# Kernel tuning notes

Hardware: AMD Instinct MI355X
Metric: run time of the kernel (lower is better)

## Reference

```python
import jax, jax.numpy as jnp
import numpy as np

N_STATE = 4      # d_state from CrossMambaFusionBlock(d_state=4)
DT_RANK = 48     # ceil(768/16), standard Mamba dt_rank='auto'
D_CONV = 4       # depthwise causal conv kernel size


def _ln(x, g, b):
    m = jnp.mean(x, axis=-1, keepdims=True)
    v = jnp.mean((x - m) ** 2, axis=-1, keepdims=True)
    return (x - m) * jax.lax.rsqrt(v + 1e-5) * g + b


def _dwconv1d(u, w, b):
    # u: (B,L,D); w: (D,1,K) depthwise causal conv along token dim L
    K = w.shape[-1]
    up = jnp.pad(jnp.transpose(u, (0, 2, 1)), ((0, 0), (0, 0), (K - 1, 0)))
    out = jax.lax.conv_general_dilated(up, w, (1,), 'VALID',
                                       feature_group_count=w.shape[0],
                                       dimension_numbers=('NCH', 'OIH', 'NCH'))
    return jnp.transpose(out, (0, 2, 1)) + b


def _pre(x, g, b, Win, Wconv, bconv, Wxp, Wdt, bdt):
    # LayerNorm -> in_proj -> depthwise conv + SiLU -> dt/B/C projections
    B_, H, W, C = x.shape
    xn = _ln(x, g, b).reshape(B_, H * W, C)
    u, z = jnp.split(xn @ Win, 2, axis=-1)              # (B,L,D) each
    u = jax.nn.silu(_dwconv1d(u, Wconv, bconv))
    dbl = u @ Wxp                                        # (B,L,R+2N)
    dtr, Bm, Cm = jnp.split(dbl, [DT_RANK, DT_RANK + N_STATE], axis=-1)
    dt = jax.nn.softplus(dtr @ Wdt + bdt)                # (B,L,D)
    return u, z, dt, Bm, Cm


def _selective_scan(u, dt, Alog, Bm, Cm, Dskip):
    # u, dt: (B,L,D); Alog: (D,N); Bm, Cm: (B,L,N)
    A = -jnp.exp(Alog)
    dA = jnp.exp(dt[..., None] * A)                      # (B,L,D,N) decay
    dBu = (dt * u)[..., None] * Bm[:, :, None, :]        # (B,L,D,N) input

    def comb(c1, c2):
        a1, h1 = c1
        a2, h2 = c2
        return a1 * a2, a2 * h1 + h2

    _, h = jax.lax.associative_scan(comb, (dA, dBu), axis=1)
    return jnp.einsum('bldn,bln->bld', h, Cm) + u * Dskip


def _forward(x1, x2,
             ln_g1, ln_b1, Win1, Wconv1, bconv1, Wxp1, Wdt1, bdt1, Alog1, Dskip1, Wout1,
             ln_g2, ln_b2, Win2, Wconv2, bconv2, Wxp2, Wdt2, bdt2, Alog2, Dskip2, Wout2):
    x1 = jnp.transpose(x1, (0, 2, 3, 1))  # BCHW -> BHWC (as in forward_features)
    x2 = jnp.transpose(x2, (0, 2, 3, 1))
    B_, H, W, C = x1.shape
    u1, z1, dt1, B1, C1 = _pre(x1, ln_g1, ln_b1, Win1, Wconv1, bconv1, Wxp1, Wdt1, bdt1)
    u2, z2, dt2, B2, C2 = _pre(x2, ln_g2, ln_b2, Win2, Wconv2, bconv2, Wxp2, Wdt2, bdt2)
    # Cross-modal fusion: each stream's SSM state is read out with the OTHER
    # stream's C projection (cross selective scan).
    y1 = _selective_scan(u1, dt1, Alog1, B1, C2, Dskip1)
    y2 = _selective_scan(u2, dt2, Alog2, B2, C1, Dskip2)
    o1 = ((y1 * jax.nn.silu(z1)) @ Wout1).reshape(B_, H, W, C)
    o2 = ((y2 * jax.nn.silu(z2)) @ Wout2).reshape(B_, H, W, C)
    return x1 + o1, x2 + o2


def setup_inputs():
    key = jax.random.key(0)
    ks = jax.random.split(key, 16)
    B_, C, H, W = 2, 768, 64, 64
    D = C  # d_inner (ssm_ratio = 1)

    def nrm(k, shape, s=0.02):
        return jax.random.normal(k, shape, jnp.float32) * s

    inp = {
        'x1': jax.random.normal(ks[0], (B_, C, H, W), jnp.float32),
        'x2': jax.random.normal(ks[1], (B_, C, H, W), jnp.float32),
    }
    for i, o in ((1, 2), (2, 8)):
        inp[f'ln_g{i}'] = jnp.ones((C,), jnp.float32)
        inp[f'ln_b{i}'] = jnp.zeros((C,), jnp.float32)
        inp[f'Win{i}'] = nrm(ks[o], (C, 2 * D))
        inp[f'Wconv{i}'] = nrm(ks[o + 1], (D, 1, D_CONV), 0.1)
        inp[f'bconv{i}'] = jnp.zeros((D,), jnp.float32)
        inp[f'Wxp{i}'] = nrm(ks[o + 2], (D, DT_RANK + 2 * N_STATE))
        inp[f'Wdt{i}'] = nrm(ks[o + 3], (DT_RANK, D), 0.05)
        inp[f'bdt{i}'] = jnp.full((D,), -4.6, jnp.float32)  # softplus -> dt ~ 0.01
        inp[f'Alog{i}'] = jnp.log(jnp.broadcast_to(
            jnp.arange(1, N_STATE + 1, dtype=jnp.float32), (D, N_STATE)))
        inp[f'Dskip{i}'] = jnp.ones((D,), jnp.float32)
        inp[f'Wout{i}'] = nrm(ks[o + 4], (D, C))
    return inp


def reference(x1, x2,
              ln_g1, ln_b1, Win1, Wconv1, bconv1, Wxp1, Wdt1, bdt1, Alog1, Dskip1, Wout1,
              ln_g2, ln_b2, Win2, Wconv2, bconv2, Wxp2, Wdt2, bdt2, Alog2, Dskip2, Wout2):
    return _forward(x1, x2,
                    ln_g1, ln_b1, Win1, Wconv1, bconv1, Wxp1, Wdt1, bdt1, Alog1, Dskip1, Wout1,
                    ln_g2, ln_b2, Win2, Wconv2, bconv2, Wxp2, Wdt2, bdt2, Alog2, Dskip2, Wout2)
```

## Files before the change

kernel.cpp:

```cpp
#include <hip/hip_runtime.h>
#include <cmath>

#define LDIM 4096
#define CDIM 768
#define BDIM 2
#define NST 4
#define RNK 48
#define CH 64
#define LC 64
#define NDT 896

typedef short bf16x8 __attribute__((ext_vector_type(8)));
typedef float f32x4 __attribute__((ext_vector_type(4)));

__device__ __forceinline__ float sigmoidf_(float x) { return 1.f / (1.f + __expf(-x)); }

__device__ __forceinline__ unsigned short f2bf(float f) {
    unsigned int u = __float_as_uint(f);
    u += 0x7fffu + ((u >> 16) & 1u);
    return (unsigned short)(u >> 16);
}
__device__ __forceinline__ float bf2f(unsigned short us) {
    unsigned int u = ((unsigned int)us) << 16;
    return __uint_as_float(u);
}

__device__ __forceinline__ void llds16(const unsigned short* g, unsigned short* l) {
    __builtin_amdgcn_global_load_lds(
        (const __attribute__((address_space(1))) unsigned int*)g,
        (__attribute__((address_space(3))) unsigned int*)l, 16, 0, 0);
}

__global__ __launch_bounds__(256) void prep_kernel(
    const float* __restrict__ x0, const float* __restrict__ x1, float* __restrict__ stats,
    const float* __restrict__ Win0, const float* __restrict__ Win1,
    const float* __restrict__ Wout0, const float* __restrict__ Wout1,
    unsigned short* __restrict__ WinT0, unsigned short* __restrict__ WinT1,
    unsigned short* __restrict__ WoutT0, unsigned short* __restrict__ WoutT1,
    const float* __restrict__ Wxp0, const float* __restrict__ Wdt0,
    const float* __restrict__ Wxp1, const float* __restrict__ Wdt1,
    unsigned short* __restrict__ Wc0, unsigned short* __restrict__ Wc1)
{
    __shared__ float smem[64 * 65];
    int bid = blockIdx.x;
    int t = threadIdx.x;

    if (bid < 256) {
        int s = bid >> 7;
        int b = (bid >> 6) & 1;
        int l0 = (bid & 63) * 64;
        int wave = t >> 6, lane = t & 63;
        const float* x = s ? x1 : x0;
        const float* xp = x + ((size_t)b * CDIM) * LDIM + l0 + lane;
        float sm = 0.f, sq = 0.f;
        int cbeg = wave * 192;
#pragma unroll
        for (int i0 = 0; i0 < 192; i0 += 16) {
            float v[16];
#pragma unroll
            for (int j = 0; j < 16; j++) v[j] = xp[(size_t)(cbeg + i0 + j) * LDIM];
#pragma unroll
            for (int j = 0; j < 16; j++) { sm += v[j]; sq += v[j] * v[j]; }
        }
        float* red = smem;
        red[(0 * 4 + wave) * 64 + lane] = sm;
        red[(1 * 4 + wave) * 64 + lane] = sq;
        __syncthreads();
        if (wave == 0) {
            float s_ = red[lane] + red[64 + lane] + red[128 + lane] + red[192 + lane];
            float q_ = red[256 + lane] + red[320 + lane] + red[384 + lane] + red[448 + lane];
            float m = s_ * (1.f / CDIM);
            float var = q_ * (1.f / CDIM) - m * m;
            int idx = s * 8192 + b * LDIM + l0 + lane;
            stats[2 * idx] = m;
            stats[2 * idx + 1] = rsqrtf(var + 1e-5f);
        }
        return;
    }
    if (bid < 1408) {
        int b2 = bid - 256;
        int bx = b2 % 24, by = (b2 / 24) % 12, z = b2 / 288;
        const float* W = (z == 0) ? Win0 : (z == 1) ? Win1 : (z == 2) ? Wout0 : Wout1;
        unsigned short* Wt = (z == 0) ? WinT0 : (z == 1) ? WinT1 : (z == 2) ? WoutT0 : WoutT1;
        const int K = CDIM;
        const int N = (z < 2) ? 2 * CDIM : CDIM;
        if (bx * 64 >= N) return;
        float (*tile)[65] = (float(*)[65])smem;
        int n0 = bx * 64, k0 = by * 64;
        int tn = t & 63, tg = t >> 6;
#pragma unroll
        for (int i = 0; i < 16; i++) {
            int kl = tg * 16 + i;
            tile[kl][tn] = W[(size_t)(k0 + kl) * N + n0 + tn];
        }
        __syncthreads();
#pragma unroll
        for (int i = 0; i < 16; i++) {
            int nl = tg * 16 + i;
            int k = k0 + tn, n = n0 + nl;
            Wt[(size_t)n * K + k] = f2bf(tile[tn][nl]);
        }
        return;
    }
    {
        int b3 = bid - 1408;
        int bx = b3 % 12, by = (b3 / 12) % 14, s = b3 / 168;
        const float* Wxp = s ? Wxp1 : Wxp0;
        const float* Wdt = s ? Wdt1 : Wdt0;
        unsigned short* WcombT = s ? Wc1 : Wc0;
        int k = bx * 64 + (t & 63);
        int n0 = by * 64;
        float wx[RNK];
#pragma unroll
        for (int r = 0; r < RNK; r++) wx[r] = Wxp[k * 56 + r];
        for (int i = (t >> 6); i < 64; i += 4) {
            int n = n0 + i;
            float val;
            if (n < CDIM) {
                float acc = 0.f;
#pragma unroll
                for (int r = 0; r < RNK; r++) acc += wx[r] * Wdt[(size_t)r * CDIM + n];
                val = acc;
            } else if (n < CDIM + 8) {
                val = Wxp[k * 56 + RNK + (n - CDIM)];
            } else {
                val = 0.f;
            }
            WcombT[(size_t)n * CDIM + k] = f2bf(val);
        }
    }
}

__global__ __launch_bounds__(256) void transpose_ln_kernel(
    const float* __restrict__ x0, const float* __restrict__ x1,
    const float* __restrict__ g0, const float* __restrict__ bb0,
    const float* __restrict__ g1, const float* __restrict__ bb1,
    const float* __restrict__ stats,
    unsigned short* __restrict__ xnb0, unsigned short* __restrict__ xnb1,
    float* __restrict__ out)
{
    __shared__ float tile[64][65];
    int t = threadIdx.x;
    int c0 = blockIdx.x * 64, l0 = blockIdx.y * 64;
    int z = blockIdx.z;
    int s = z >> 1, b = z & 1;
    const float* x = s ? x1 : x0;
    const float* g = s ? g1 : g0;
    const float* bb = s ? bb1 : bb0;
    unsigned short* xnb = s ? xnb1 : xnb0;
    int lane16 = t & 15, cg = t >> 4;
#pragma unroll
    for (int i = 0; i < 4; i++) {
        int cl = cg + 16 * i;
        f32x4 v = *(const f32x4*)&x[((size_t)(b * CDIM + c0 + cl)) * LDIM + l0 + lane16 * 4];
#pragma unroll
        for (int j = 0; j < 4; j++) tile[cl][lane16 * 4 + j] = v[j];
    }
    __syncthreads();
    const size_t SZ = (size_t)BDIM * LDIM * CDIM;
    int tl = t & 63, tg = t >> 6;
#pragma unroll
    for (int i = 0; i < 16; i++) {
        int ll = tg * 16 + i;
        int l = l0 + ll, c = c0 + tl;
        float v = tile[tl][ll];
        int sidx = s * 8192 + b * LDIM + l;
        float m = stats[sidx * 2], rs = stats[sidx * 2 + 1];
        size_t o = ((size_t)(b * LDIM + l)) * CDIM + c;
        out[(size_t)s * SZ + o] = v;
        xnb[o] = f2bf((v - m) * rs * g[c] + bb[c]);
    }
}

__global__ __launch_bounds__(512, 2) void gemm_mfma(
    const unsigned short* __restrict__ A0, const unsigned short* __restrict__ A1,
    const unsigned short* __restrict__ Bt0, const unsigned short* __restrict__ Bt1,
    void* __restrict__ C0, void* __restrict__ C1, int ldc, int K, int epi,
    const float* __restrict__ bias0, const float* __restrict__ bias1,
    float* __restrict__ D0, float* __restrict__ D1)
{
    const unsigned short* A = blockIdx.z ? A1 : A0;
    const unsigned short* Bt = blockIdx.z ? Bt1 : Bt0;
    void* C = blockIdx.z ? C1 : C0;
    const float* bias = blockIdx.z ? bias1 : bias0;
    float* D = blockIdx.z ? D1 : D0;

    __shared__ unsigned short As[2][256 * 64];
    __shared__ unsigned short Bs[2][128 * 64];

    const int tid = threadIdx.x;
    const int wave = tid >> 6, lane = tid & 63;
    const int row0 = blockIdx.x * 256, col0 = blockIdx.y * 128;
    const int wm = (wave >> 1) * 64;
    const int wn = (wave & 1) * 64;
    f32x4 acc[4][4] = {};

    const int rs = tid >> 3;
    const int kcg = (tid & 7) ^ (rs & 7);
    const unsigned short* gA = A + (size_t)(row0 + rs) * K + kcg * 8;
    const unsigned short* gB = Bt + (size_t)(col0 + rs) * K + kcg * 8;
    const size_t rK = (size_t)64 * K;
    const int fr = lane & 15, fc = lane >> 4;

    auto ldfrag = [&](const unsigned short* s, int row, int kc) -> bf16x8 {
        return *(const bf16x8*)&s[row * 64 + ((kc ^ (row & 7)) << 3)];
    };

#define GSTAGE(nb, kt)                                                       \
    do {                                                                     \
        const unsigned short* a_ = gA + (size_t)(kt) * 64;                   \
        const unsigned short* b_ = gB + (size_t)(kt) * 64;                   \
        unsigned short* al = &As[nb][wave * 512];                            \
        unsigned short* bl = &Bs[nb][wave * 512];                            \
        _Pragma("unroll")                                                    \
        for (int r_ = 0; r_ < 4; r_++) llds16(a_ + r_ * rK, al + r_ * 4096); \
        _Pragma("unroll")                                                    \
        for (int r_ = 0; r_ < 2; r_++) llds16(b_ + r_ * rK, bl + r_ * 4096); \
    } while (0)

    const int NKT = K / 64;
    GSTAGE(0, 0);
    __builtin_amdgcn_s_waitcnt(0xF70);
    __builtin_amdgcn_s_barrier();

    for (int kt = 0; kt < NKT; kt++) {
        const int cur = kt & 1;
        if (kt + 1 < NKT) GSTAGE(cur ^ 1, kt + 1);
        const unsigned short* as = As[cur];
        const unsigned short* bs = Bs[cur];
#pragma unroll
        for (int ks = 0; ks < 2; ks++) {
            bf16x8 af[4], bf[4];
#pragma unroll
            for (int mi = 0; mi < 4; mi++) af[mi] = ldfrag(as, wm + mi * 16 + fr, ks * 4 + fc);
#pragma unroll
            for (int nj = 0; nj < 4; nj++) bf[nj] = ldfrag(bs, wn + nj * 16 + fr, ks * 4 + fc);
#pragma unroll
            for (int mi = 0; mi < 4; mi++)
#pragma unroll
                for (int nj = 0; nj < 4; nj++)
                    acc[mi][nj] = __builtin_amdgcn_mfma_f32_16x16x32_bf16(af[mi], bf[nj], acc[mi][nj], 0, 0, 0);
        }
        __builtin_amdgcn_s_waitcnt(0xF70);
        __builtin_amdgcn_s_barrier();
    }
#undef GSTAGE

    const int cr = (lane >> 4) * 4, cc = lane & 15;
#pragma unroll
    for (int mi = 0; mi < 4; mi++)
#pragma unroll
        for (int nj = 0; nj < 4; nj++) {
            int col = col0 + wn + nj * 16 + cc;
#pragma unroll
            for (int r = 0; r < 4; r++) {
                int row = row0 + wm + mi * 16 + cr + r;
                float v = acc[mi][nj][r];
                if (epi == 1) {
                    float* Cf = (float*)C;
                    size_t o = (size_t)row * ldc + col;
                    Cf[o] = v + Cf[o];
                } else if (epi == 2) {
                    if (col < CDIM) {
                        v += bias[col];
                        v = (v > 20.f) ? v : __logf(1.f + __expf(v));
                        ((unsigned short*)C)[(size_t)row * ldc + col] = f2bf(v);
                    } else if (col < CDIM + 8) {
                        D[(size_t)row * 8 + (col - CDIM)] = v;
                    }
                } else {
                    ((unsigned short*)C)[(size_t)row * ldc + col] = f2bf(v);
                }
            }
        }
}

__global__ __launch_bounds__(256) void conv_silu_kernel(
    const unsigned short* __restrict__ uzb0, const unsigned short* __restrict__ uzb1,
    const float* __restrict__ w0, const float* __restrict__ bc0,
    const float* __restrict__ w1, const float* __restrict__ bc1,
    unsigned short* __restrict__ ub0, unsigned short* __restrict__ ub1)
{
    int s = blockIdx.y;
    const unsigned short* uzb = s ? uzb1 : uzb0;
    const float* w = s ? w1 : w0;
    const float* bc = s ? bc1 : bc0;
    unsigned short* ub = s ? ub1 : ub0;
    int idx = blockIdx.x * 256 + threadIdx.x;
    int d8 = (idx % 96) * 8;
    int bl = idx / 96;
    int l = bl & (LDIM - 1);

    float wr[8][4];
#pragma unroll
    for (int q = 0; q < 8; q++) {
        f32x4 wv = *(const f32x4*)&w[(d8 + q) * 4];
#pragma unroll
        for (int k = 0; k < 4; k++) wr[q][k] = wv[k];
    }
    float acc[8];
    f32x4 b0 = *(const f32x4*)&bc[d8];
    f32x4 b1 = *(const f32x4*)&bc[d8 + 4];
#pragma unroll
    for (int q = 0; q < 4; q++) { acc[q] = b0[q]; acc[4 + q] = b1[q]; }

#pragma unroll
    for (int k = 0; k < 4; k++) {
        int ls = l - 3 + k;
        if (ls >= 0) {
            bf16x8 uv = *(const bf16x8*)&uzb[(size_t)(bl - 3 + k) * (2 * CDIM) + d8];
#pragma unroll
            for (int q = 0; q < 8; q++)
                acc[q] += bf2f((unsigned short)uv[q]) * wr[q][k];
        }
    }
    bf16x8 ov;
#pragma unroll
    for (int q = 0; q < 8; q++) {
        float v = acc[q];
        ov[q] = (short)f2bf(v * sigmoidf_(v));
    }
    *(bf16x8*)&ub[(size_t)bl * CDIM + d8] = ov;
}

__global__ __launch_bounds__(256) void scan_phaseA(
    const unsigned short* __restrict__ u0, const unsigned short* __restrict__ dt0,
    const float* __restrict__ dbl0, const float* __restrict__ Alog0,
    const unsigned short* __restrict__ u1, const unsigned short* __restrict__ dt1,
    const float* __restrict__ dbl1, const float* __restrict__ Alog1,
    float* __restrict__ agg)
{
    int idx = blockIdx.x * 256 + threadIdx.x;
    int d = idx % CDIM;
    int t1 = idx / CDIM;
    int c = t1 % CH;
    int t2 = t1 / CH;
    int b = t2 & 1;
    int s = t2 >> 1;
    const unsigned short* u = s ? u1 : u0;
    const unsigned short* dt = s ? dt1 : dt0;
    const float* dbl = s ? dbl1 : dbl0;
    const float* Alog = s ? Alog1 : Alog0;
    float A[4];
#pragma unroll
    for (int n = 0; n < 4; n++) A[n] = -__expf(Alog[d * 4 + n]);
    float h[4] = {0, 0, 0, 0}, aa[4] = {1, 1, 1, 1};
    int rowb = b * LDIM + c * LC;
    for (int t = 0; t < LC; t++) {
        int row = rowb + t;
        float dtv = bf2f(dt[(size_t)row * CDIM + d]);
        float uv = bf2f(u[(size_t)row * CDIM + d]);
        float du = dtv * uv;
        const float* bm = dbl + (size_t)row * 8;
#pragma unroll
        for (int n = 0; n < 4; n++) {
            float dA = __expf(dtv * A[n]);
            h[n] = dA * h[n] + du * bm[n];
            aa[n] *= dA;
        }
    }
    float* o = agg + (size_t)idx * 8;
#pragma unroll
    for (int n = 0; n < 4; n++) { o[n] = aa[n]; o[4 + n] = h[n]; }
}

__global__ __launch_bounds__(256) void scan_phaseB(const float* __restrict__ agg,
                                                   float* __restrict__ hinit)
{
    int idx = blockIdx.x * 256 + threadIdx.x;
    int d = idx % CDIM;
    int sb = idx / CDIM;
    float st[4] = {0, 0, 0, 0};
    for (int c = 0; c < CH; c++) {
        size_t base = ((size_t)sb * CH + c) * CDIM + d;
        const float* a = agg + base * 8;
        float* hi = hinit + base * 4;
#pragma unroll
        for (int n = 0; n < 4; n++) hi[n] = st[n];
#pragma unroll
        for (int n = 0; n < 4; n++) st[n] = a[n] * st[n] + a[4 + n];
    }
}

__global__ __launch_bounds__(256) void scan_phaseC(
    const unsigned short* __restrict__ u0, const unsigned short* __restrict__ dt0,
    const unsigned short* __restrict__ uzb0, const float* __restrict__ dbl0,
    const float* __restrict__ Alog0, const float* __restrict__ Dsk0, unsigned short* __restrict__ g0,
    const unsigned short* __restrict__ u1, const unsigned short* __restrict__ dt1,
    const unsigned short* __restrict__ uzb1, const float* __restrict__ dbl1,
    const float* __restrict__ Alog1, const float* __restrict__ Dsk1, unsigned short* __restrict__ g1,
    const float* __restrict__ hinit)
{
    int idx = blockIdx.x * 256 + threadIdx.x;
    int d = idx % CDIM;
    int t1 = idx / CDIM;
    int c = t1 % CH;
    int t2 = t1 / CH;
    int b = t2 & 1;
    int s = t2 >> 1;
    const unsigned short* u = s ? u1 : u0;
    const unsigned short* dt = s ? dt1 : dt0;
    const unsigned short* uzb = s ? uzb1 : uzb0;
    const float* dbl = s ? dbl1 : dbl0;
    const float* dblO = s ? dbl0 : dbl1;
    const float* Alog = s ? Alog1 : Alog0;
    const float* Dsk = s ? Dsk1 : Dsk0;
    unsigned short* gated = s ? g1 : g0;
    float A[4];
#pragma unroll
    for (int n = 0; n < 4; n++) A[n] = -__expf(Alog[d * 4 + n]);
    float Dv = Dsk[d];
    float h[4];
    const float* hi = hinit + (size_t)idx * 4;
#pragma unroll
    for (int n = 0; n < 4; n++) h[n] = hi[n];
    int rowb = b * LDIM + c * LC;
    for (int t = 0; t < LC; t++) {
        int row = rowb + t;
        float dtv = bf2f(dt[(size_t)row * CDIM + d]);
        float uv = bf2f(u[(size_t)row * CDIM + d]);
        float du = dtv * uv;
        const float* bm = dbl + (size_t)row * 8;
        const float* cm = dblO + (size_t)row * 8 + 4;
        float y = 0.f;
#pragma unroll
        for (int n = 0; n < 4; n++) {
            float dA = __expf(dtv * A[n]);
            h[n] = dA * h[n] + du * bm[n];
            y += h[n] * cm[n];
        }
        y += uv * Dv;
        float zv = bf2f(uzb[(size_t)row * (2 * CDIM) + CDIM + d]);
        gated[(size_t)row * CDIM + d] = f2bf(y * (zv * sigmoidf_(zv)));
    }
}

extern "C" void kernel_launch(void* const* d_in, const int* in_sizes, int n_in,
                              void* d_out, int out_size, void* d_ws, size_t ws_size,
                              hipStream_t stream)
{
    const float* x[2] = {(const float*)d_in[0], (const float*)d_in[1]};
    const float *ln_g[2], *ln_b[2], *Win[2], *Wconv[2], *bconv[2], *Wxp[2],
        *Wdt[2], *bdt[2], *Alog[2], *Dskip[2], *Wout[2];
    for (int s = 0; s < 2; s++) {
        int base = 2 + s * 11;
        ln_g[s] = (const float*)d_in[base + 0];
        ln_b[s] = (const float*)d_in[base + 1];
        Win[s] = (const float*)d_in[base + 2];
        Wconv[s] = (const float*)d_in[base + 3];
        bconv[s] = (const float*)d_in[base + 4];
        Wxp[s] = (const float*)d_in[base + 5];
        Wdt[s] = (const float*)d_in[base + 6];
        bdt[s] = (const float*)d_in[base + 7];
        Alog[s] = (const float*)d_in[base + 8];
        Dskip[s] = (const float*)d_in[base + 9];
        Wout[s] = (const float*)d_in[base + 10];
    }

    const int M = BDIM * LDIM;
    char* base = (char*)d_ws;
    auto alloc = [&](size_t bytes) {
        char* p = base;
        base += (bytes + 255) & ~(size_t)255;
        return p;
    };
    unsigned short* uzb[2] = {(unsigned short*)alloc((size_t)M * 1536 * 2),
                              (unsigned short*)alloc((size_t)M * 1536 * 2)};
    unsigned short* dtb[2] = {(unsigned short*)alloc((size_t)M * CDIM * 2),
                              (unsigned short*)alloc((size_t)M * CDIM * 2)};
    unsigned short* ub[2] = {(unsigned short*)alloc((size_t)M * CDIM * 2),
                             (unsigned short*)alloc((size_t)M * CDIM * 2)};
    unsigned short* xnb[2] = {(unsigned short*)alloc((size_t)M * CDIM * 2),
                              (unsigned short*)alloc((size_t)M * CDIM * 2)};
    float* dbl[2] = {(float*)alloc((size_t)M * 8 * 4), (float*)alloc((size_t)M * 8 * 4)};
    unsigned short* WinT[2] = {(unsigned short*)alloc(1536 * 768 * 2),
                               (unsigned short*)alloc(1536 * 768 * 2)};
    unsigned short* WoutT[2] = {(unsigned short*)alloc(768 * 768 * 2),
                                (unsigned short*)alloc(768 * 768 * 2)};
    unsigned short* WcombT[2] = {(unsigned short*)alloc((size_t)NDT * 768 * 2),
                                 (unsigned short*)alloc((size_t)NDT * 768 * 2)};
    float* agg = (float*)alloc((size_t)2 * BDIM * CH * CDIM * 8 * 4);
    float* hinit = (float*)alloc((size_t)2 * BDIM * CH * CDIM * 4 * 4);
    float* stats = (float*)alloc((size_t)2 * M * 2 * 4);

    dim3 blk(256);
    dim3 blk512(512);
    const size_t SZ = (size_t)BDIM * LDIM * CDIM;

    prep_kernel<<<dim3(1744), blk, 0, stream>>>(
        x[0], x[1], stats,
        Win[0], Win[1], Wout[0], Wout[1], WinT[0], WinT[1], WoutT[0], WoutT[1],
        Wxp[0], Wdt[0], Wxp[1], Wdt[1], WcombT[0], WcombT[1]);

    transpose_ln_kernel<<<dim3(CDIM / 64, LDIM / 64, 4), blk, 0, stream>>>(
        x[0], x[1], ln_g[0], ln_b[0], ln_g[1], ln_b[1], stats, xnb[0], xnb[1], (float*)d_out);

    gemm_mfma<<<dim3(M / 256, 1536 / 128, 2), blk512, 0, stream>>>(
        xnb[0], xnb[1], WinT[0], WinT[1], uzb[0], uzb[1], 2 * CDIM, CDIM, 3,
        nullptr, nullptr, nullptr, nullptr);

    conv_silu_kernel<<<dim3((M * CDIM / 8) / 256, 2), blk, 0, stream>>>(
        uzb[0], uzb[1], Wconv[0], bconv[0], Wconv[1], bconv[1], ub[0], ub[1]);

    gemm_mfma<<<dim3(M / 256, NDT / 128, 2), blk512, 0, stream>>>(
        ub[0], ub[1], WcombT[0], WcombT[1], dtb[0], dtb[1], CDIM, CDIM, 2,
        bdt[0], bdt[1], dbl[0], dbl[1]);

    scan_phaseA<<<dim3((2 * BDIM * CH * CDIM) / 256), blk, 0, stream>>>(
        ub[0], dtb[0], dbl[0], Alog[0], ub[1], dtb[1], dbl[1], Alog[1], agg);
    scan_phaseB<<<dim3((2 * BDIM * CDIM) / 256), blk, 0, stream>>>(agg, hinit);
    scan_phaseC<<<dim3((2 * BDIM * CH * CDIM) / 256), blk, 0, stream>>>(
        ub[0], dtb[0], uzb[0], dbl[0], Alog[0], Dskip[0], xnb[0],
        ub[1], dtb[1], uzb[1], dbl[1], Alog[1], Dskip[1], xnb[1], hinit);

    float* out = (float*)d_out;
    gemm_mfma<<<dim3(M / 256, CDIM / 128, 2), blk512, 0, stream>>>(
        xnb[0], xnb[1], WoutT[0], WoutT[1], out, out + SZ, CDIM, CDIM, 1,
        nullptr, nullptr, nullptr, nullptr);
}
```

Before: 475.3 us.

## Retile MFMA GEMM to 128xBN blocks with three-stage LDS pipeline

```diff
diff --git a/kernel.cpp b/kernel.cpp
--- a/kernel.cpp
+++ b/kernel.cpp
@@ -172,7 +172,8 @@
     }
 }
 
-__global__ __launch_bounds__(512, 2) void gemm_mfma(
+template <int BN>
+__global__ __launch_bounds__(256, 2) void gemm_mfma(
     const unsigned short* __restrict__ A0, const unsigned short* __restrict__ A1,
     const unsigned short* __restrict__ Bt0, const unsigned short* __restrict__ Bt1,
     void* __restrict__ C0, void* __restrict__ C1, int ldc, int K, int epi,
@@ -185,72 +186,70 @@
     const float* bias = blockIdx.z ? bias1 : bias0;
     float* D = blockIdx.z ? D1 : D0;
 
-    __shared__ unsigned short As[2][256 * 64];
-    __shared__ unsigned short Bs[2][128 * 64];
+    constexpr int NJ = BN / 32;
+    constexpr int RB = BN / 64;
+    constexpr int LPT = 2 + RB;
+    constexpr int WCNT = 0xF70 | LPT;
+
+    __shared__ unsigned short As[3][128 * 32];
+    __shared__ unsigned short Bs[3][BN * 32];
 
     const int tid = threadIdx.x;
     const int wave = tid >> 6, lane = tid & 63;
-    const int row0 = blockIdx.x * 256, col0 = blockIdx.y * 128;
+    const int row0 = blockIdx.x * 128, col0 = blockIdx.y * BN;
     const int wm = (wave >> 1) * 64;
-    const int wn = (wave & 1) * 64;
-    f32x4 acc[4][4] = {};
-
-    const int rs = tid >> 3;
-    const int kcg = (tid & 7) ^ (rs & 7);
+    const int wn = (wave & 1) * (BN / 2);
+    f32x4 acc[4][NJ] = {};
+
+    const int rs = tid >> 2;
+    const int kcg = (tid & 3) ^ (rs & 3);
     const unsigned short* gA = A + (size_t)(row0 + rs) * K + kcg * 8;
     const unsigned short* gB = Bt + (size_t)(col0 + rs) * K + kcg * 8;
-    const size_t rK = (size_t)64 * K;
+    const size_t r64K = (size_t)64 * K;
     const int fr = lane & 15, fc = lane >> 4;
 
-    auto ldfrag = [&](const unsigned short* s, int row, int kc) -> bf16x8 {
-        return *(const bf16x8*)&s[row * 64 + ((kc ^ (row & 7)) << 3)];
+    auto ldfrag = [&](const unsigned short* s, int row) -> bf16x8 {
+        return *(const bf16x8*)&s[row * 32 + ((fc ^ (row & 3)) << 3)];
     };
 
-#define GSTAGE(nb, kt)                                                       \
-    do {                                                                     \
-        const unsigned short* a_ = gA + (size_t)(kt) * 64;                   \
-        const unsigned short* b_ = gB + (size_t)(kt) * 64;                   \
-        unsigned short* al = &As[nb][wave * 512];                            \
-        unsigned short* bl = &Bs[nb][wave * 512];                            \
-        _Pragma("unroll")                                                    \
-        for (int r_ = 0; r_ < 4; r_++) llds16(a_ + r_ * rK, al + r_ * 4096); \
-        _Pragma("unroll")                                                    \
-        for (int r_ = 0; r_ < 2; r_++) llds16(b_ + r_ * rK, bl + r_ * 4096); \
-    } while (0)
-
-    const int NKT = K / 64;
+    auto GSTAGE = [&](int nb, int kt) {
+        const unsigned short* a_ = gA + (size_t)kt * 32;
+        const unsigned short* b_ = gB + (size_t)kt * 32;
+        unsigned short* al = &As[nb][wave * 512];
+        unsigned short* bl = &Bs[nb][wave * 512];
+#pragma unroll
+        for (int r_ = 0; r_ < 2; r_++) llds16(a_ + r_ * r64K, al + r_ * 2048);
+#pragma unroll
+        for (int r_ = 0; r_ < RB; r_++) llds16(b_ + r_ * r64K, bl + r_ * 2048);
+    };
+
+    const int NIT = K / 32;
     GSTAGE(0, 0);
-    __builtin_amdgcn_s_waitcnt(0xF70);
-    __builtin_amdgcn_s_barrier();
-
-    for (int kt = 0; kt < NKT; kt++) {
-        const int cur = kt & 1;
-        if (kt + 1 < NKT) GSTAGE(cur ^ 1, kt + 1);
-        const unsigned short* as = As[cur];
-        const unsigned short* bs = Bs[cur];
-#pragma unroll
-        for (int ks = 0; ks < 2; ks++) {
-            bf16x8 af[4], bf[4];
-#pragma unroll
-            for (int mi = 0; mi < 4; mi++) af[mi] = ldfrag(as, wm + mi * 16 + fr, ks * 4 + fc);
-#pragma unroll
-            for (int nj = 0; nj < 4; nj++) bf[nj] = ldfrag(bs, wn + nj * 16 + fr, ks * 4 + fc);
-#pragma unroll
-            for (int mi = 0; mi < 4; mi++)
-#pragma unroll
-                for (int nj = 0; nj < 4; nj++)
-                    acc[mi][nj] = __builtin_amdgcn_mfma_f32_16x16x32_bf16(af[mi], bf[nj], acc[mi][nj], 0, 0, 0);
-        }
-        __builtin_amdgcn_s_waitcnt(0xF70);
+    GSTAGE(1, 1);
+    for (int i = 0; i < NIT; i++) {
+        if (i < NIT - 1) __builtin_amdgcn_s_waitcnt(WCNT);
+        else __builtin_amdgcn_s_waitcnt(0xF70);
         __builtin_amdgcn_s_barrier();
-    }
-#undef GSTAGE
+        if (i + 2 < NIT) GSTAGE((i + 2) % 3, i + 2);
+        const unsigned short* as = As[i % 3];
+        const unsigned short* bs = Bs[i % 3];
+        bf16x8 af[4], bf[NJ];
+#pragma unroll
+        for (int mi = 0; mi < 4; mi++) af[mi] = ldfrag(as, wm + mi * 16 + fr);
+#pragma unroll
+        for (int nj = 0; nj < NJ; nj++) bf[nj] = ldfrag(bs, wn + nj * 16 + fr);
+#pragma unroll
+        for (int mi = 0; mi < 4; mi++)
+#pragma unroll
+            for (int nj = 0; nj < NJ; nj++)
+                acc[mi][nj] = __builtin_amdgcn_mfma_f32_16x16x32_bf16(af[mi], bf[nj], acc[mi][nj], 0, 0, 0);
+    }
 
     const int cr = (lane >> 4) * 4, cc = lane & 15;
 #pragma unroll
     for (int mi = 0; mi < 4; mi++)
 #pragma unroll
-        for (int nj = 0; nj < 4; nj++) {
+        for (int nj = 0; nj < NJ; nj++) {
             int col = col0 + wn + nj * 16 + cc;
 #pragma unroll
             for (int r = 0; r < 4; r++) {
@@ -484,7 +483,6 @@
     float* stats = (float*)alloc((size_t)2 * M * 2 * 4);
 
     dim3 blk(256);
-    dim3 blk512(512);
     const size_t SZ = (size_t)BDIM * LDIM * CDIM;
 
     prep_kernel<<<dim3(1744), blk, 0, stream>>>(
@@ -495,14 +493,14 @@
     transpose_ln_kernel<<<dim3(CDIM / 64, LDIM / 64, 4), blk, 0, stream>>>(
         x[0], x[1], ln_g[0], ln_b[0], ln_g[1], ln_b[1], stats, xnb[0], xnb[1], (float*)d_out);
 
-    gemm_mfma<<<dim3(M / 256, 1536 / 128, 2), blk512, 0, stream>>>(
+    gemm_mfma<192><<<dim3(M / 128, 1536 / 192, 2), blk, 0, stream>>>(
         xnb[0], xnb[1], WinT[0], WinT[1], uzb[0], uzb[1], 2 * CDIM, CDIM, 3,
         nullptr, nullptr, nullptr, nullptr);
 
     conv_silu_kernel<<<dim3((M * CDIM / 8) / 256, 2), blk, 0, stream>>>(
         uzb[0], uzb[1], Wconv[0], bconv[0], Wconv[1], bconv[1], ub[0], ub[1]);
 
-    gemm_mfma<<<dim3(M / 256, NDT / 128, 2), blk512, 0, stream>>>(
+    gemm_mfma<128><<<dim3(M / 128, NDT / 128, 2), blk, 0, stream>>>(
         ub[0], ub[1], WcombT[0], WcombT[1], dtb[0], dtb[1], CDIM, CDIM, 2,
         bdt[0], bdt[1], dbl[0], dbl[1]);
 
@@ -514,7 +512,7 @@
         ub[1], dtb[1], uzb[1], dbl[1], Alog[1], Dskip[1], xnb[1], hinit);
 
     float* out = (float*)d_out;
-    gemm_mfma<<<dim3(M / 256, CDIM / 128, 2), blk512, 0, stream>>>(
+    gemm_mfma<192><<<dim3(M / 128, CDIM / 192, 2), blk, 0, stream>>>(
         xnb[0], xnb[1], WoutT[0], WoutT[1], out, out + SZ, CDIM, CDIM, 1,
         nullptr, nullptr, nullptr, nullptr);
 }
```

Result: slower. 503.9 us (+6.0%).
